# Kernel optimization log

Measured on AMD Instinct MI355X. Metric: run time of the kernel, lower is better.

Reference implementation:

```python
import jax, jax.numpy as jnp
import numpy as np

DIM = 1024

def setup_inputs() -> dict:
    key = jax.random.key(0)
    ks = jax.random.split(key, 6)
    B, T, D = 8, 2048, DIM
    s = 1.0 / np.sqrt(D)
    x = jax.random.normal(ks[0], (B, T, D), dtype=jnp.float32)
    Wq = jax.random.normal(ks[1], (D, D), dtype=jnp.float32) * s
    Wk = jax.random.normal(ks[2], (D, D), dtype=jnp.float32) * s
    Wv = jax.random.normal(ks[3], (D, D), dtype=jnp.float32) * s
    Wp = jax.random.normal(ks[4], (D, D), dtype=jnp.float32) * s
    bp = jax.random.normal(ks[5], (D,), dtype=jnp.float32) * 0.01
    return {"x": x, "Wq": Wq, "Wk": Wk, "Wv": Wv, "Wp": Wp, "bp": bp}

def reference(x, Wq, Wk, Wv, Wp, bp):
    # x: [b, t, d]; weights stored as [d_in, d_out] (torch Linear applies x @ W.T;
    # here we bake the transpose into the stored matrix).
    scale = x.shape[-1] ** (-0.5)
    q = jnp.einsum('btd,de->bte', x, Wq)
    k = jnp.einsum('btd,de->bte', x, Wk)
    v = jnp.einsum('btd,de->bte', x, Wv)
    attn = jax.nn.softmax(jnp.einsum('btd,bTd->btT', q, k) * scale, axis=-1)
    out = jnp.einsum('btT,bTd->btd', attn, v)
    return jnp.einsum('btd,de->bte', out, Wp) + bp
```

## Files before the change

kernel.cpp:

```cpp
#include <hip/hip_runtime.h>


typedef _Float16 half_t;
typedef _Float16 half8 __attribute__((ext_vector_type(8)));
typedef float floatx4 __attribute__((ext_vector_type(4)));

#define GLD16(gp, lp)                                                          \
    __builtin_amdgcn_global_load_lds(                                          \
        (const __attribute__((address_space(1))) void*)(gp),                   \
        (__attribute__((address_space(3))) void*)(lp), 16, 0, 0)

#define WAIT_VM0()  asm volatile("s_waitcnt vmcnt(0)" ::: "memory")
#define BARRIER()   do { asm volatile("" ::: "memory");                        \
                         __builtin_amdgcn_s_barrier();                         \
                         asm volatile("" ::: "memory"); } while (0)

template<int EPI>
__global__ __launch_bounds__(256, 2)
void gemm16(const half_t* __restrict__ A, const half_t* __restrict__ B,
            void* __restrict__ Cv, void* __restrict__ C2, void* __restrict__ C3,
            const float* __restrict__ bias, int K, int lda, int ldb, int ldc,
            long long bsA, long long bsB, long long bsC)
{
    __shared__ half_t As[2 * 128 * 32];
    __shared__ half_t Bs[2 * 128 * 32];

    const int tid  = threadIdx.x;
    const int lane = tid & 63;
    const int wid  = tid >> 6;
    const int wr   = (wid >> 1) * 64;
    const int wc   = (wid & 1) * 64;
    const long long z = blockIdx.z;
    const int rowBase = blockIdx.y * 128;
    const int colBase = blockIdx.x * 128;

    const int srow = wid * 32 + (lane >> 2);
    const int scol = (lane & 3) * 8;

    const half_t* ga0 = A + z * bsA + (long long)(rowBase + srow) * lda + scol;
    const half_t* ga1 = ga0 + 16LL * lda;
    const half_t* gb0 = B + z * bsB + (long long)(colBase + srow) * ldb + scol;
    const half_t* gb1 = gb0 + 16LL * ldb;
    const int lso0 = (wid * 32) * 32;
    const int lso1 = (wid * 32 + 16) * 32;

    floatx4 acc[4][4];
    #pragma unroll
    for (int m = 0; m < 4; ++m)
        #pragma unroll
        for (int n = 0; n < 4; ++n)
            #pragma unroll
            for (int j = 0; j < 4; ++j) acc[m][n][j] = 0.0f;

    const int fr = lane & 15;
    const int fk = (lane >> 4) * 8;
    const int nIter = K >> 5;

    GLD16(ga0, &As[lso0]);
    GLD16(ga1, &As[lso1]);
    GLD16(gb0, &Bs[lso0]);
    GLD16(gb1, &Bs[lso1]);
    WAIT_VM0();
    BARRIER();

    for (int it = 0; it < nIter; ++it) {
        const int cur = (it & 1) * 4096;
        const int nxt = 4096 - cur;
        if (it + 1 < nIter) {
            const int kk = (it + 1) << 5;
            GLD16(ga0 + kk, &As[nxt + lso0]);
            GLD16(ga1 + kk, &As[nxt + lso1]);
            GLD16(gb0 + kk, &Bs[nxt + lso0]);
            GLD16(gb1 + kk, &Bs[nxt + lso1]);
        }

        half8 af[4], bf[4];
        #pragma unroll
        for (int m = 0; m < 4; ++m)
            af[m] = *(const half8*)&As[cur + (wr + m * 16 + fr) * 32 + fk];
        #pragma unroll
        for (int n = 0; n < 4; ++n)
            bf[n] = *(const half8*)&Bs[cur + (wc + n * 16 + fr) * 32 + fk];
        #pragma unroll
        for (int m = 0; m < 4; ++m)
            #pragma unroll
            for (int n = 0; n < 4; ++n)
                acc[m][n] = __builtin_amdgcn_mfma_f32_16x16x32_f16(af[m], bf[n], acc[m][n], 0, 0, 0);

        WAIT_VM0();
        BARRIER();
    }

    const int ecol = lane & 15;
    const int q4   = (lane >> 4) * 4;
    #pragma unroll
    for (int m = 0; m < 4; ++m) {
        #pragma unroll
        for (int n = 0; n < 4; ++n) {
            const int gcol = colBase + wc + n * 16 + ecol;
            #pragma unroll
            for (int r = 0; r < 4; ++r) {
                const int grow = rowBase + wr + m * 16 + q4 + r;
                float v = acc[m][n][r];
                if (EPI == 0) {
                    ((half_t*)Cv)[z * bsC + (long long)grow * ldc + gcol] = (half_t)v;
                } else if (EPI == 1) {
                    ((float*)Cv)[(long long)grow * ldc + gcol] = v + bias[gcol];
                } else {
                    const int mat = colBase >> 10;
                    const int c   = gcol & 1023;
                    if (mat == 0) {
                        ((half_t*)Cv)[(long long)grow * 1024 + c] = (half_t)(v * 0.03125f);
                    } else if (mat == 1) {
                        ((half_t*)C2)[(long long)grow * 1024 + c] = (half_t)v;
                    } else {
                        const long long bb = grow >> 11;
                        const long long tt = grow & 2047;
                        ((half_t*)C3)[bb * (1024LL * 2048) + (long long)c * 2048 + tt] = (half_t)v;
                    }
                }
            }
        }
    }
}

__global__ __launch_bounds__(256)
void cast16(const float* __restrict__ x, half_t* __restrict__ y)
{
    const long long i = ((long long)blockIdx.x * 256 + threadIdx.x) * 8;
    floatx4 a = *(const floatx4*)(x + i);
    floatx4 b = *(const floatx4*)(x + i + 4);
    half8 h;
    #pragma unroll
    for (int j = 0; j < 4; ++j) { h[j] = (half_t)a[j]; h[j + 4] = (half_t)b[j]; }
    *(half8*)(y + i) = h;
}

__global__ __launch_bounds__(256)
void cast_transpose4(const float* __restrict__ W0, const float* __restrict__ W1,
                     const float* __restrict__ W2, const float* __restrict__ W3,
                     half_t* __restrict__ WT)
{
    const float* W = (blockIdx.z == 0) ? W0 : (blockIdx.z == 1) ? W1
                   : (blockIdx.z == 2) ? W2 : W3;
    half_t* O = WT + (long long)blockIdx.z * 1024 * 1024;
    __shared__ float t[32][33];
    const int bx = blockIdx.x * 32, by = blockIdx.y * 32;
    const int tx = threadIdx.x, ty = threadIdx.y;
    #pragma unroll
    for (int i = 0; i < 32; i += 8)
        t[ty + i][tx] = W[(long long)(by + ty + i) * 1024 + bx + tx];
    __syncthreads();
    #pragma unroll
    for (int i = 0; i < 32; i += 8)
        O[(long long)(bx + ty + i) * 1024 + by + tx] = (half_t)t[tx][ty + i];
}

__global__ __launch_bounds__(256)
void softmax_rows(half_t* __restrict__ S)
{
    const long long base = (long long)blockIdx.x * 2048;
    const int t = threadIdx.x;
    half8 h = *(const half8*)(S + base + t * 8);
    float v[8];
    #pragma unroll
    for (int i = 0; i < 8; ++i) v[i] = (float)h[i];
    float m = -3.0e38f;
    #pragma unroll
    for (int i = 0; i < 8; ++i) m = fmaxf(m, v[i]);
    #pragma unroll
    for (int off = 32; off > 0; off >>= 1) m = fmaxf(m, __shfl_down(m, off));
    __shared__ float redm[4], reds[4];
    const int lane = t & 63, wid = t >> 6;
    if (lane == 0) redm[wid] = m;
    __syncthreads();
    const float M = fmaxf(fmaxf(redm[0], redm[1]), fmaxf(redm[2], redm[3]));
    float s = 0.f;
    #pragma unroll
    for (int i = 0; i < 8; ++i) { v[i] = __expf(v[i] - M); s += v[i]; }
    #pragma unroll
    for (int off = 32; off > 0; off >>= 1) s += __shfl_down(s, off);
    if (lane == 0) reds[wid] = s;
    __syncthreads();
    const float inv = 1.0f / (reds[0] + reds[1] + reds[2] + reds[3]);
    #pragma unroll
    for (int i = 0; i < 8; ++i) h[i] = (half_t)(v[i] * inv);
    *(half8*)(S + base + t * 8) = h;
}

extern "C" void kernel_launch(void* const* d_in, const int* in_sizes, int n_in,
                              void* d_out, int out_size, void* d_ws, size_t ws_size,
                              hipStream_t stream)
{
    const float* x  = (const float*)d_in[0];
    const float* Wq = (const float*)d_in[1];
    const float* Wk = (const float*)d_in[2];
    const float* Wv = (const float*)d_in[3];
    const float* Wp = (const float*)d_in[4];
    const float* bp = (const float*)d_in[5];
    float* out = (float*)d_out;

    char* ws = (char*)d_ws;
    const long long MB = 1024LL * 1024LL;
    half_t* WqkvT = (half_t*)(ws + 0 * MB);
    half_t* WpT   = (half_t*)(ws + 6 * MB);
    half_t* q     = (half_t*)(ws + 8 * MB);
    half_t* k     = (half_t*)(ws + 40 * MB);
    half_t* vT    = (half_t*)(ws + 72 * MB);
    half_t* x16   = (half_t*)(ws + 104 * MB);
    half_t* S     = (half_t*)(ws + 104 * MB);

    dim3 blk(256);
    cast16<<<8192, blk, 0, stream>>>(x, x16);
    cast_transpose4<<<dim3(32, 32, 4), dim3(32, 8), 0, stream>>>(Wq, Wk, Wv, Wp, WqkvT);

    gemm16<2><<<dim3(24, 128, 1), blk, 0, stream>>>(
        x16, WqkvT, q, k, vT, nullptr, 1024, 1024, 1024, 0, 0, 0, 0);

    gemm16<0><<<dim3(16, 16, 8), blk, 0, stream>>>(
        q, k, S, nullptr, nullptr, nullptr, 1024, 1024, 1024, 2048,
        2048LL * 1024, 2048LL * 1024, 2048LL * 2048);

    softmax_rows<<<8 * 2048, blk, 0, stream>>>(S);

    gemm16<0><<<dim3(8, 16, 8), blk, 0, stream>>>(
        S, vT, q, nullptr, nullptr, nullptr, 2048, 2048, 2048, 1024,
        2048LL * 2048, 1024LL * 2048, 2048LL * 1024);

    gemm16<1><<<dim3(8, 128, 1), blk, 0, stream>>>(
        q, WpT, out, nullptr, nullptr, bp, 1024, 1024, 1024, 1024, 0, 0, 0);
}
```

Before: 549.5 us.

## Use two waves per GEMM block with 64x128 warp tiles

Changes the GEMM block from four waves (each computing a 64x64 tile) to two waves, each computing a 64x128 tile of the same 128x128 block output. Each wave now holds 32 accumulator fragments and loads 8 B fragments per k-step, which raises MFMA work per LDS read. Each thread also issues four global-to-LDS loads per operand instead of two. The cost is roughly doubled accumulator register pressure and fewer waves per CU for hiding latency, since launch_bounds still asks for only 2 blocks.

```diff
diff --git a/kernel.cpp b/kernel.cpp
--- a/kernel.cpp
+++ b/kernel.cpp
@@ -16,7 +16,7 @@
                          asm volatile("" ::: "memory"); } while (0)
 
 template<int EPI>
-__global__ __launch_bounds__(256, 2)
+__global__ __launch_bounds__(128, 2)
 void gemm16(const half_t* __restrict__ A, const half_t* __restrict__ B,
             void* __restrict__ Cv, void* __restrict__ C2, void* __restrict__ C3,
             const float* __restrict__ bias, int K, int lda, int ldb, int ldc,
@@ -28,27 +28,23 @@
     const int tid  = threadIdx.x;
     const int lane = tid & 63;
     const int wid  = tid >> 6;
-    const int wr   = (wid >> 1) * 64;
-    const int wc   = (wid & 1) * 64;
+    const int wr   = wid * 64;
     const long long z = blockIdx.z;
     const int rowBase = blockIdx.y * 128;
     const int colBase = blockIdx.x * 128;
 
-    const int srow = wid * 32 + (lane >> 2);
+    const int srow = wid * 64 + (lane >> 2);
     const int scol = (lane & 3) * 8;
 
-    const half_t* ga0 = A + z * bsA + (long long)(rowBase + srow) * lda + scol;
-    const half_t* ga1 = ga0 + 16LL * lda;
-    const half_t* gb0 = B + z * bsB + (long long)(colBase + srow) * ldb + scol;
-    const half_t* gb1 = gb0 + 16LL * ldb;
-    const int lso0 = (wid * 32) * 32;
-    const int lso1 = (wid * 32 + 16) * 32;
-
-    floatx4 acc[4][4];
+    const half_t* gA = A + z * bsA + (long long)(rowBase + srow) * lda + scol;
+    const half_t* gB = B + z * bsB + (long long)(colBase + srow) * ldb + scol;
+    const int lso = (wid * 64) * 32;
+
+    floatx4 acc[4][8];
     #pragma unroll
     for (int m = 0; m < 4; ++m)
         #pragma unroll
-        for (int n = 0; n < 4; ++n)
+        for (int n = 0; n < 8; ++n)
             #pragma unroll
             for (int j = 0; j < 4; ++j) acc[m][n][j] = 0.0f;
 
@@ -56,10 +52,11 @@
     const int fk = (lane >> 4) * 8;
     const int nIter = K >> 5;
 
-    GLD16(ga0, &As[lso0]);
-    GLD16(ga1, &As[lso1]);
-    GLD16(gb0, &Bs[lso0]);
-    GLD16(gb1, &Bs[lso1]);
+    #pragma unroll
+    for (int j = 0; j < 4; ++j) {
+        GLD16(gA + (long long)(16 * j) * lda, &As[lso + (16 * j) * 32]);
+        GLD16(gB + (long long)(16 * j) * ldb, &Bs[lso + (16 * j) * 32]);
+    }
     WAIT_VM0();
     BARRIER();
 
@@ -68,23 +65,24 @@
         const int nxt = 4096 - cur;
         if (it + 1 < nIter) {
             const int kk = (it + 1) << 5;
-            GLD16(ga0 + kk, &As[nxt + lso0]);
-            GLD16(ga1 + kk, &As[nxt + lso1]);
-            GLD16(gb0 + kk, &Bs[nxt + lso0]);
-            GLD16(gb1 + kk, &Bs[nxt + lso1]);
+            #pragma unroll
+            for (int j = 0; j < 4; ++j) {
+                GLD16(gA + (long long)(16 * j) * lda + kk, &As[nxt + lso + (16 * j) * 32]);
+                GLD16(gB + (long long)(16 * j) * ldb + kk, &Bs[nxt + lso + (16 * j) * 32]);
+            }
         }
 
-        half8 af[4], bf[4];
+        half8 af[4], bf[8];
         #pragma unroll
         for (int m = 0; m < 4; ++m)
             af[m] = *(const half8*)&As[cur + (wr + m * 16 + fr) * 32 + fk];
         #pragma unroll
-        for (int n = 0; n < 4; ++n)
-            bf[n] = *(const half8*)&Bs[cur + (wc + n * 16 + fr) * 32 + fk];
+        for (int n = 0; n < 8; ++n)
+            bf[n] = *(const half8*)&Bs[cur + (n * 16 + fr) * 32 + fk];
         #pragma unroll
         for (int m = 0; m < 4; ++m)
             #pragma unroll
-            for (int n = 0; n < 4; ++n)
+            for (int n = 0; n < 8; ++n)
                 acc[m][n] = __builtin_amdgcn_mfma_f32_16x16x32_f16(af[m], bf[n], acc[m][n], 0, 0, 0);
 
         WAIT_VM0();
@@ -96,8 +94,8 @@
     #pragma unroll
     for (int m = 0; m < 4; ++m) {
         #pragma unroll
-        for (int n = 0; n < 4; ++n) {
-            const int gcol = colBase + wc + n * 16 + ecol;
+        for (int n = 0; n < 8; ++n) {
+            const int gcol = colBase + n * 16 + ecol;
             #pragma unroll
             for (int r = 0; r < 4; ++r) {
                 const int grow = rowBase + wr + m * 16 + q4 + r;
@@ -210,8 +208,8 @@
     half_t* x16   = (half_t*)(ws + 104 * MB);
     half_t* S     = (half_t*)(ws + 104 * MB);
 
-    dim3 blk(256);
-    cast16<<<8192, blk, 0, stream>>>(x, x16);
+    dim3 blk(128);
+    cast16<<<8192, dim3(256), 0, stream>>>(x, x16);
     cast_transpose4<<<dim3(32, 32, 4), dim3(32, 8), 0, stream>>>(Wq, Wk, Wv, Wp, WqkvT);
 
     gemm16<2><<<dim3(24, 128, 1), blk, 0, stream>>>(
@@ -221,7 +219,7 @@
         q, k, S, nullptr, nullptr, nullptr, 1024, 1024, 1024, 2048,
         2048LL * 1024, 2048LL * 1024, 2048LL * 2048);
 
-    softmax_rows<<<8 * 2048, blk, 0, stream>>>(S);
+    softmax_rows<<<8 * 2048, dim3(256), 0, stream>>>(S);
 
     gemm16<0><<<dim3(8, 16, 8), blk, 0, stream>>>(
         S, vT, q, nullptr, nullptr, nullptr, 2048, 2048, 2048, 1024,
```

New measurement: 577.8 us. 1.05x slower.

## Triple-buffer GEMM loads, swizzle LDS, remap blocks across XCDs

Applied to the files above, without the earlier changes.

Moves the fp16 GEMM from a double to a triple LDS buffer with prefetch distance two and partial vmcnt waits, so global loads overlap more with MFMA work. It adds an XOR swizzle on LDS chunk placement to reduce bank conflicts on fragment reads. It remaps block indices so neighbouring tiles stay on the same XCD for L2 reuse, and raises launch bounds to 4 blocks per CU. The larger LDS footprint may cap real occupancy, and the tighter register bound could cause spills.

```diff
diff --git a/kernel.cpp b/kernel.cpp
--- a/kernel.cpp
+++ b/kernel.cpp
@@ -10,36 +10,45 @@
         (const __attribute__((address_space(1))) void*)(gp),                   \
         (__attribute__((address_space(3))) void*)(lp), 16, 0, 0)
 
-#define WAIT_VM0()  asm volatile("s_waitcnt vmcnt(0)" ::: "memory")
+#define WAIT_VM(N)  asm volatile("s_waitcnt vmcnt(" #N ")" ::: "memory")
 #define BARRIER()   do { asm volatile("" ::: "memory");                        \
                          __builtin_amdgcn_s_barrier();                         \
                          asm volatile("" ::: "memory"); } while (0)
 
 template<int EPI>
-__global__ __launch_bounds__(256, 2)
+__global__ __launch_bounds__(256, 4)
 void gemm16(const half_t* __restrict__ A, const half_t* __restrict__ B,
             void* __restrict__ Cv, void* __restrict__ C2, void* __restrict__ C3,
             const float* __restrict__ bias, int K, int lda, int ldb, int ldc,
             long long bsA, long long bsB, long long bsC)
 {
-    __shared__ half_t As[2 * 128 * 32];
-    __shared__ half_t Bs[2 * 128 * 32];
+    __shared__ half_t As[3 * 128 * 32];
+    __shared__ half_t Bs[3 * 128 * 32];
+
+    const int gx = gridDim.x, gy = gridDim.y;
+    const int lin  = blockIdx.x + gx * (blockIdx.y + gy * blockIdx.z);
+    const int xcd  = lin & 7;
+    const int slot = lin >> 3;
+    const int ppx  = (gy * gridDim.z) >> 3;
+    const int gp   = xcd * ppx + slot / gx;
+    const int bx   = slot % gx;
+    const int by   = gp % gy;
+    const long long z = gp / gy;
 
     const int tid  = threadIdx.x;
     const int lane = tid & 63;
     const int wid  = tid >> 6;
     const int wr   = (wid >> 1) * 64;
     const int wc   = (wid & 1) * 64;
-    const long long z = blockIdx.z;
-    const int rowBase = blockIdx.y * 128;
-    const int colBase = blockIdx.x * 128;
-
-    const int srow = wid * 32 + (lane >> 2);
-    const int scol = (lane & 3) * 8;
-
-    const half_t* ga0 = A + z * bsA + (long long)(rowBase + srow) * lda + scol;
+    const int rowBase = by * 128;
+    const int colBase = bx * 128;
+
+    const int lrow = lane >> 2;
+    const int scol = (((lane & 3) ^ ((lane >> 3) & 3))) * 8;
+
+    const half_t* ga0 = A + z * bsA + (long long)(rowBase + wid * 32 + lrow) * lda + scol;
     const half_t* ga1 = ga0 + 16LL * lda;
-    const half_t* gb0 = B + z * bsB + (long long)(colBase + srow) * ldb + scol;
+    const half_t* gb0 = B + z * bsB + (long long)(colBase + wid * 32 + lrow) * ldb + scol;
     const half_t* gb1 = gb0 + 16LL * ldb;
     const int lso0 = (wid * 32) * 32;
     const int lso1 = (wid * 32 + 16) * 32;
@@ -52,43 +61,51 @@
             #pragma unroll
             for (int j = 0; j < 4; ++j) acc[m][n][j] = 0.0f;
 
-    const int fr = lane & 15;
-    const int fk = (lane >> 4) * 8;
+    const int fr  = lane & 15;
+    const int fks = (((lane >> 4) ^ ((lane >> 1) & 3))) * 8;
     const int nIter = K >> 5;
 
-    GLD16(ga0, &As[lso0]);
-    GLD16(ga1, &As[lso1]);
-    GLD16(gb0, &Bs[lso0]);
-    GLD16(gb1, &Bs[lso1]);
-    WAIT_VM0();
+    GLD16(ga0, &As[0 * 4096 + lso0]);
+    GLD16(ga1, &As[0 * 4096 + lso1]);
+    GLD16(gb0, &Bs[0 * 4096 + lso0]);
+    GLD16(gb1, &Bs[0 * 4096 + lso1]);
+    GLD16(ga0 + 32, &As[1 * 4096 + lso0]);
+    GLD16(ga1 + 32, &As[1 * 4096 + lso1]);
+    GLD16(gb0 + 32, &Bs[1 * 4096 + lso0]);
+    GLD16(gb1 + 32, &Bs[1 * 4096 + lso1]);
+    WAIT_VM(4);
     BARRIER();
 
+    int cur = 0;
     for (int it = 0; it < nIter; ++it) {
-        const int cur = (it & 1) * 4096;
-        const int nxt = 4096 - cur;
-        if (it + 1 < nIter) {
-            const int kk = (it + 1) << 5;
-            GLD16(ga0 + kk, &As[nxt + lso0]);
-            GLD16(ga1 + kk, &As[nxt + lso1]);
-            GLD16(gb0 + kk, &Bs[nxt + lso0]);
-            GLD16(gb1 + kk, &Bs[nxt + lso1]);
+        if (it + 2 < nIter) {
+            int pf = cur + 2; if (pf >= 3) pf -= 3;
+            const int kk = (it + 2) << 5;
+            GLD16(ga0 + kk, &As[pf * 4096 + lso0]);
+            GLD16(ga1 + kk, &As[pf * 4096 + lso1]);
+            GLD16(gb0 + kk, &Bs[pf * 4096 + lso0]);
+            GLD16(gb1 + kk, &Bs[pf * 4096 + lso1]);
         }
 
+        const int co = cur * 4096;
         half8 af[4], bf[4];
         #pragma unroll
         for (int m = 0; m < 4; ++m)
-            af[m] = *(const half8*)&As[cur + (wr + m * 16 + fr) * 32 + fk];
+            af[m] = *(const half8*)&As[co + (wr + m * 16 + fr) * 32 + fks];
         #pragma unroll
         for (int n = 0; n < 4; ++n)
-            bf[n] = *(const half8*)&Bs[cur + (wc + n * 16 + fr) * 32 + fk];
+            bf[n] = *(const half8*)&Bs[co + (wc + n * 16 + fr) * 32 + fks];
         #pragma unroll
         for (int m = 0; m < 4; ++m)
             #pragma unroll
             for (int n = 0; n < 4; ++n)
                 acc[m][n] = __builtin_amdgcn_mfma_f32_16x16x32_f16(af[m], bf[n], acc[m][n], 0, 0, 0);
 
-        WAIT_VM0();
-        BARRIER();
+        if (it + 1 < nIter) {
+            if (it + 2 < nIter) { WAIT_VM(4); } else { WAIT_VM(0); }
+            BARRIER();
+        }
+        ++cur; if (cur >= 3) cur = 0;
     }
 
     const int ecol = lane & 15;
```

New measurement: 556.1 us. Within noise of the previous version (+1.2%).
